# Performance work log

Hardware: AMD Instinct MI355X
Metric: run time of the kernel (lower is better)

Reference implementation:

```python
import jax, jax.numpy as jnp
import numpy as np

N, D, K = 32768, 128, 32
EPS = 1e-8  # torch.cosine_similarity default eps


def setup_inputs() -> dict:
    key = jax.random.key(0)
    k1, k2, k3, k4, k5 = jax.random.split(key, 5)
    # xavier_normal_ std = sqrt(2/(fan_in+fan_out)); torch treats dims (-2,-1) as (fan_in, fan_out)
    std_w = (2.0 / (D + D)) ** 0.5
    std_v = (2.0 / (2 * D + 1)) ** 0.5
    return {
        "x_1": jax.random.normal(k1, (N, D), dtype=jnp.float32),
        "x_2": jax.random.normal(k2, (N, D), dtype=jnp.float32),
        "W1": jax.random.normal(k3, (K, D, D), dtype=jnp.float32) * std_w,
        "W2": jax.random.normal(k4, (K, D, D), dtype=jnp.float32) * std_w,
        "V": jax.random.normal(k5, (K, 2 * D, 1), dtype=jnp.float32) * std_v,
        "b": jnp.zeros((K,), dtype=jnp.float32),
    }


def reference(x_1, x_2, W1, W2, V, b):
    # Batched bilinear transforms: [N, K, D]
    x1t = jnp.einsum("nd,kde->nke", x_1, W1)
    x2t = jnp.einsum("nd,kde->nke", x_2, W2)
    # Cosine similarity along last dim (torch semantics: clamp norms at eps)
    dot = jnp.sum(x1t * x2t, axis=-1)                     # [N, K]
    n1 = jnp.maximum(jnp.linalg.norm(x1t, axis=-1), EPS)  # [N, K]
    n2 = jnp.maximum(jnp.linalg.norm(x2t, axis=-1), EPS)
    part1 = dot / (n1 * n2)
    # part2 = cat([x1, x2]) @ V[k]  -> [N, K]
    xcat = jnp.concatenate([x_1, x_2], axis=-1)           # [N, 2D]
    part2 = jnp.einsum("nf,kf->nk", xcat, V[:, :, 0])
    return jax.nn.relu(part1 + part2 + b)
```

## Files before the change

### kernel.cpp

```cpp
#include <hip/hip_runtime.h>
#include <cstdint>
#include <cstddef>

#define DD 128
#define KK 32
constexpr float EPS = 1e-8f;

typedef __bf16 bf16x8 __attribute__((ext_vector_type(8)));
typedef float f32x4 __attribute__((ext_vector_type(4)));

__device__ __forceinline__ unsigned short f2bf(float x) {
    union { float f; uint32_t u; } v; v.f = x;
    uint32_t r = v.u + 0x7FFFu + ((v.u >> 16) & 1u);
    return (unsigned short)(r >> 16);
}
__device__ __forceinline__ __bf16 f2bf16(float x) {
    unsigned short u = f2bf(x);
    __bf16 r; __builtin_memcpy(&r, &u, 2); return r;
}
__device__ __forceinline__ uint4 pack8(float4 a, float4 b) {
    uint4 o;
    o.x = (uint32_t)f2bf(a.x) | ((uint32_t)f2bf(a.y) << 16);
    o.y = (uint32_t)f2bf(a.z) | ((uint32_t)f2bf(a.w) << 16);
    o.z = (uint32_t)f2bf(b.x) | ((uint32_t)f2bf(b.y) << 16);
    o.w = (uint32_t)f2bf(b.z) | ((uint32_t)f2bf(b.w) << 16);
    return o;
}

template <int CTRL>
__device__ __forceinline__ float dpp_fold(float x) {
    union { float f; int i; } u, r;
    u.f = x;
    r.i = __builtin_amdgcn_update_dpp(0, u.i, CTRL, 0xF, 0xF, false);
    return x + r.f;
}
__device__ __forceinline__ f32x4 fold4(f32x4 v) {
    #pragma unroll
    for (int c = 0; c < 4; ++c) {
        float x = v[c];
        x = dpp_fold<0xB1>(x);
        x = dpp_fold<0x4E>(x);
        v[c] = x;
    }
    return v;
}

__global__ __launch_bounds__(256) void prep_kernel(
    const float* __restrict__ x1, const float* __restrict__ x2,
    const float* __restrict__ W1, const float* __restrict__ W2,
    __bf16* __restrict__ X1f, __bf16* __restrict__ X2f,
    __bf16* __restrict__ W1f, __bf16* __restrict__ W2f,
    int cvt_half, int wf_half)
{
    __shared__ float tile[16][132];
    int bb = blockIdx.x;
    if (bb < 2 * cvt_half) {
        const float* src; __bf16* dst;
        if (bb >= cvt_half) { src = x2; dst = X2f; bb -= cvt_half; }
        else                { src = x1; dst = X1f; }
        const int rg = bb;
        {
            const int row = threadIdx.x >> 4;
            const int c8  = (threadIdx.x & 15) * 8;
            const float* p = src + (size_t)(rg * 16 + row) * DD + c8;
            float4 f0 = *reinterpret_cast<const float4*>(p);
            float4 f1 = *reinterpret_cast<const float4*>(p + 4);
            *reinterpret_cast<float4*>(&tile[row][c8])     = f0;
            *reinterpret_cast<float4*>(&tile[row][c8 + 4]) = f1;
        }
        __syncthreads();
        {
            const int mm = threadIdx.x & 15;
            const int c  = threadIdx.x >> 4;
            float4 a = *reinterpret_cast<float4*>(&tile[mm][c * 8]);
            float4 b = *reinterpret_cast<float4*>(&tile[mm][c * 8 + 4]);
            size_t off = (size_t)rg * 2048 + (size_t)c * 128 + (size_t)mm * 8;
            *reinterpret_cast<uint4*>(dst + off) = pack8(a, b);
        }
    } else {
        bb -= 2 * cvt_half;
        const float* W; __bf16* Wf;
        if (bb >= wf_half) { W = W2; Wf = W2f; bb -= wf_half; }
        else               { W = W1; Wf = W1f; }
        int idx = bb * 256 + threadIdx.x;
        int mm = idx & 15;
        int c  = (idx >> 4) & 15;
        int eg = (idx >> 8) & 7;
        int k  = idx >> 11;
        const float* Wk = W + (size_t)k * DD * DD;
        int e = eg * 16 + mm;
        float4 a, b;
        a.x = Wk[(size_t)(c * 8 + 0) * DD + e];
        a.y = Wk[(size_t)(c * 8 + 1) * DD + e];
        a.z = Wk[(size_t)(c * 8 + 2) * DD + e];
        a.w = Wk[(size_t)(c * 8 + 3) * DD + e];
        b.x = Wk[(size_t)(c * 8 + 4) * DD + e];
        b.y = Wk[(size_t)(c * 8 + 5) * DD + e];
        b.z = Wk[(size_t)(c * 8 + 6) * DD + e];
        b.w = Wk[(size_t)(c * 8 + 7) * DD + e];
        size_t off = ((size_t)(k * 8 + eg)) * 2048 + (size_t)c * 128 + (size_t)mm * 8;
        *reinterpret_cast<uint4*>(Wf + off) = pack8(a, b);
    }
}

__global__ __launch_bounds__(256, 2) void ntn_main(
    const __bf16* __restrict__ X1f, const __bf16* __restrict__ X2f,
    const __bf16* __restrict__ W1f, const __bf16* __restrict__ W2f,
    const float* __restrict__ V, const float* __restrict__ bias,
    float* __restrict__ out, int grp_per_xcd)
{
    __shared__ __align__(16) float sRedAll[8][3][2][4][40];
    __shared__ __align__(16) float sP2[8][2][2][16];

    const int b    = blockIdx.x;
    const int xcd  = b & 7;
    const int k    = (b >> 3) & 31;
    const int grpN = xcd * grp_per_xcd + (b >> 8);
    const int tid  = threadIdx.x;
    const int wave = tid >> 6;
    const int lane = tid & 63;
    const int m    = lane & 15;
    const int quad = lane >> 4;
    const int rh   = wave & 1;
    const int eh   = wave >> 1;

    const size_t nOut = (size_t)grpN * 256 + tid;
    const float bk  = bias[k];

    const __bf16* W1p = W1f + (size_t)k * 16384;
    const __bf16* W2p = W2f + (size_t)k * 16384;

    bf16x8 Bc[2][4][4];
    #pragma unroll
    for (int ks = 0; ks < 4; ++ks)
        #pragma unroll
        for (int et = 0; et < 4; ++et) {
            const size_t boff = (size_t)(eh * 4 + et) * 2048 + ks * 512 + lane * 8;
            Bc[0][ks][et] = *reinterpret_cast<const bf16x8*>(W1p + boff);
            Bc[1][ks][et] = *reinterpret_cast<const bf16x8*>(W2p + boff);
        }

    bf16x8 Vb[4];
    {
        const float* Vk = V + (size_t)k * 256 + eh * 128 + quad * 8;
        #pragma unroll
        for (int ks = 0; ks < 4; ++ks) {
            float4 v0 = *reinterpret_cast<const float4*>(Vk + ks * 32);
            float4 v1 = *reinterpret_cast<const float4*>(Vk + ks * 32 + 4);
            bf16x8 t;
            t[0] = f2bf16(v0.x); t[1] = f2bf16(v0.y);
            t[2] = f2bf16(v0.z); t[3] = f2bf16(v0.w);
            t[4] = f2bf16(v1.x); t[5] = f2bf16(v1.y);
            t[6] = f2bf16(v1.z); t[7] = f2bf16(v1.w);
            if (m != 0) {
                #pragma unroll
                for (int j = 0; j < 8; ++j) t[j] = (__bf16)0.0f;
            }
            Vb[ks] = t;
        }
    }

    const int rg0 = grpN * 16;
    const size_t lane8 = (size_t)lane * 8;

    bf16x8 a1[4], a2[4];
    {
        const size_t ab = (size_t)(rg0 + rh) * 2048 + lane8;
        #pragma unroll
        for (int ks = 0; ks < 4; ++ks) {
            a1[ks] = *reinterpret_cast<const bf16x8*>(X1f + ab + ks * 512);
            a2[ks] = *reinterpret_cast<const bf16x8*>(X2f + ab + ks * 512);
        }
    }

    #pragma unroll
    for (int g = 0; g < 8; ++g) {
        f32x4 acc[2][4];
        #pragma unroll
        for (int mat = 0; mat < 2; ++mat)
            #pragma unroll
            for (int et = 0; et < 4; ++et) acc[mat][et] = f32x4{0.f, 0.f, 0.f, 0.f};
        f32x4 accv = {0.f, 0.f, 0.f, 0.f};

        __builtin_amdgcn_s_setprio(1);
        #pragma unroll
        for (int ks = 0; ks < 4; ++ks) {
            #pragma unroll
            for (int et = 0; et < 4; ++et) {
                acc[0][et] = __builtin_amdgcn_mfma_f32_16x16x32_bf16(a1[ks], Bc[0][ks][et], acc[0][et], 0, 0, 0);
                acc[1][et] = __builtin_amdgcn_mfma_f32_16x16x32_bf16(a2[ks], Bc[1][ks][et], acc[1][et], 0, 0, 0);
            }
        }
        if (eh == 0) {
            #pragma unroll
            for (int ks = 0; ks < 4; ++ks)
                accv = __builtin_amdgcn_mfma_f32_16x16x32_bf16(a1[ks], Vb[ks], accv, 0, 0, 0);
        } else {
            #pragma unroll
            for (int ks = 0; ks < 4; ++ks)
                accv = __builtin_amdgcn_mfma_f32_16x16x32_bf16(a2[ks], Vb[ks], accv, 0, 0, 0);
        }
        __builtin_amdgcn_s_setprio(0);

        if (g < 7) {
            const size_t ab = (size_t)(rg0 + (g + 1) * 2 + rh) * 2048 + lane8;
            #pragma unroll
            for (int ks = 0; ks < 4; ++ks) {
                a1[ks] = *reinterpret_cast<const bf16x8*>(X1f + ab + ks * 512);
                a2[ks] = *reinterpret_cast<const bf16x8*>(X2f + ab + ks * 512);
            }
        }

        f32x4 pd = {0.f, 0.f, 0.f, 0.f};
        f32x4 q1 = {0.f, 0.f, 0.f, 0.f};
        f32x4 q2 = {0.f, 0.f, 0.f, 0.f};
        #pragma unroll
        for (int et = 0; et < 4; ++et) {
            f32x4 c1 = acc[0][et];
            f32x4 c2 = acc[1][et];
            pd += c1 * c2;
            q1 += c1 * c1;
            q2 += c2 * c2;
        }
        pd = fold4(pd);
        q1 = fold4(q1);
        q2 = fold4(q2);

        if ((m & 3) == 0) {
            const int grp = m >> 2;
            const int rb  = rh * 16 + quad * 4;
            *reinterpret_cast<f32x4*>(&sRedAll[g][0][eh][grp][rb]) = pd;
            *reinterpret_cast<f32x4*>(&sRedAll[g][1][eh][grp][rb]) = q1;
            *reinterpret_cast<f32x4*>(&sRedAll[g][2][eh][grp][rb]) = q2;
        }
        if (m == 0) {
            *reinterpret_cast<f32x4*>(&sP2[g][eh][rh][quad * 4]) = accv;
        }
    }

    __syncthreads();

    {
        const int tile = tid >> 5;
        const int row  = tid & 31;
        const int rowh = row >> 4;
        const int rowl = row & 15;
        float dot = 0.f, s1 = 0.f, s2 = 0.f;
        #pragma unroll
        for (int e2 = 0; e2 < 2; ++e2)
            #pragma unroll
            for (int gg = 0; gg < 4; ++gg) {
                dot += sRedAll[tile][0][e2][gg][row];
                s1  += sRedAll[tile][1][e2][gg][row];
                s2  += sRedAll[tile][2][e2][gg][row];
            }
        float p2v = sP2[tile][0][rowh][rowl] + sP2[tile][1][rowh][rowl];
        float n1 = fmaxf(sqrtf(s1), EPS);
        float n2 = fmaxf(sqrtf(s2), EPS);
        float tot = dot / (n1 * n2) + p2v + bk;
        out[nOut * KK + k] = fmaxf(tot, 0.f);
    }
}

extern "C" void kernel_launch(void* const* d_in, const int* in_sizes, int n_in,
                              void* d_out, int out_size, void* d_ws, size_t ws_size,
                              hipStream_t stream) {
    const float* x1 = (const float*)d_in[0];
    const float* x2 = (const float*)d_in[1];
    const float* W1 = (const float*)d_in[2];
    const float* W2 = (const float*)d_in[3];
    const float* V  = (const float*)d_in[4];
    const float* b  = (const float*)d_in[5];
    float* out = (float*)d_out;

    const int N = in_sizes[0] / DD;

    __bf16* X1f = (__bf16*)d_ws;
    __bf16* X2f = X1f + (size_t)N * DD;
    __bf16* W1f = X2f + (size_t)N * DD;
    __bf16* W2f = W1f + (size_t)KK * DD * DD;

    const int cvt_half = N / 16;
    const int wf_half  = KK * DD * DD / 8 / 256;
    prep_kernel<<<2 * cvt_half + 2 * wf_half, 256, 0, stream>>>(
        x1, x2, W1, W2, X1f, X2f, W1f, W2f, cvt_half, wf_half);

    const int groups = N / 256;
    ntn_main<<<groups * KK, 256, 0, stream>>>(X1f, X2f, W1f, W2f, V, b, out,
                                              groups / 8);
}
```

Before: 167.6 us.

## Compute V projection once in prep kernel instead of per-k in main kernel

The concatenated-input projection against V was computed inside the main kernel for every k-block, re-running the same MFMA on each input tile 32 times with only one useful column. It now runs once per 16-row tile in the prep kernel, which writes two partial planes (x1 and x2 halves) of an N×K float buffer that the main kernel reads and sums. This removes MFMA work, V loads and shared-memory traffic from the hot kernel. The cost is an extra global write and read of N×K×2 floats, plus more workspace.

```diff
diff --git a/kernel.cpp b/kernel.cpp
--- a/kernel.cpp
+++ b/kernel.cpp
@@ -48,16 +48,18 @@
 __global__ __launch_bounds__(256) void prep_kernel(
     const float* __restrict__ x1, const float* __restrict__ x2,
     const float* __restrict__ W1, const float* __restrict__ W2,
+    const float* __restrict__ V,
     __bf16* __restrict__ X1f, __bf16* __restrict__ X2f,
     __bf16* __restrict__ W1f, __bf16* __restrict__ W2f,
+    float* __restrict__ p2,
     int cvt_half, int wf_half)
 {
     __shared__ float tile[16][132];
     int bb = blockIdx.x;
     if (bb < 2 * cvt_half) {
-        const float* src; __bf16* dst;
-        if (bb >= cvt_half) { src = x2; dst = X2f; bb -= cvt_half; }
-        else                { src = x1; dst = X1f; }
+        const float* src; __bf16* dst; int half;
+        if (bb >= cvt_half) { src = x2; dst = X2f; half = 1; bb -= cvt_half; }
+        else                { src = x1; dst = X1f; half = 0; }
         const int rg = bb;
         {
             const int row = threadIdx.x >> 4;
@@ -76,6 +78,42 @@
             float4 b = *reinterpret_cast<float4*>(&tile[mm][c * 8 + 4]);
             size_t off = (size_t)rg * 2048 + (size_t)c * 128 + (size_t)mm * 8;
             *reinterpret_cast<uint4*>(dst + off) = pack8(a, b);
+        }
+        const int wave = threadIdx.x >> 6;
+        if (wave < 2) {
+            const int lane = threadIdx.x & 63;
+            const int m    = lane & 15;
+            const int quad = lane >> 4;
+            const int ct   = wave;
+            bf16x8 a[4], bf[4];
+            #pragma unroll
+            for (int ks = 0; ks < 4; ++ks) {
+                float4 a0 = *reinterpret_cast<float4*>(&tile[m][ks * 32 + quad * 8]);
+                float4 a1 = *reinterpret_cast<float4*>(&tile[m][ks * 32 + quad * 8 + 4]);
+                bf16x8 t;
+                t[0] = f2bf16(a0.x); t[1] = f2bf16(a0.y);
+                t[2] = f2bf16(a0.z); t[3] = f2bf16(a0.w);
+                t[4] = f2bf16(a1.x); t[5] = f2bf16(a1.y);
+                t[6] = f2bf16(a1.z); t[7] = f2bf16(a1.w);
+                a[ks] = t;
+                const float* Vp = V + (size_t)(ct * 16 + m) * 256 + half * 128 + ks * 32 + quad * 8;
+                float4 v0 = *reinterpret_cast<const float4*>(Vp);
+                float4 v1 = *reinterpret_cast<const float4*>(Vp + 4);
+                bf16x8 u;
+                u[0] = f2bf16(v0.x); u[1] = f2bf16(v0.y);
+                u[2] = f2bf16(v0.z); u[3] = f2bf16(v0.w);
+                u[4] = f2bf16(v1.x); u[5] = f2bf16(v1.y);
+                u[6] = f2bf16(v1.z); u[7] = f2bf16(v1.w);
+                bf[ks] = u;
+            }
+            f32x4 acc = {0.f, 0.f, 0.f, 0.f};
+            #pragma unroll
+            for (int ks = 0; ks < 4; ++ks)
+                acc = __builtin_amdgcn_mfma_f32_16x16x32_bf16(a[ks], bf[ks], acc, 0, 0, 0);
+            float* p2h = p2 + (size_t)half * (size_t)cvt_half * 16 * KK;
+            #pragma unroll
+            for (int reg = 0; reg < 4; ++reg)
+                p2h[(size_t)(rg * 16 + quad * 4 + reg) * KK + ct * 16 + m] = acc[reg];
         }
     } else {
         bb -= 2 * cvt_half;
@@ -106,11 +144,10 @@
 __global__ __launch_bounds__(256, 2) void ntn_main(
     const __bf16* __restrict__ X1f, const __bf16* __restrict__ X2f,
     const __bf16* __restrict__ W1f, const __bf16* __restrict__ W2f,
-    const float* __restrict__ V, const float* __restrict__ bias,
-    float* __restrict__ out, int grp_per_xcd)
+    const float* __restrict__ p2, const float* __restrict__ bias,
+    float* __restrict__ out, int grp_per_xcd, int plane)
 {
     __shared__ __align__(16) float sRedAll[8][3][2][4][40];
-    __shared__ __align__(16) float sP2[8][2][2][16];
 
     const int b    = blockIdx.x;
     const int xcd  = b & 7;
@@ -125,6 +162,7 @@
     const int eh   = wave >> 1;
 
     const size_t nOut = (size_t)grpN * 256 + tid;
+    const float p2v = p2[nOut * KK + k] + p2[nOut * KK + k + (size_t)plane];
     const float bk  = bias[k];
 
     const __bf16* W1p = W1f + (size_t)k * 16384;
@@ -140,26 +178,6 @@
             Bc[1][ks][et] = *reinterpret_cast<const bf16x8*>(W2p + boff);
         }
 
-    bf16x8 Vb[4];
-    {
-        const float* Vk = V + (size_t)k * 256 + eh * 128 + quad * 8;
-        #pragma unroll
-        for (int ks = 0; ks < 4; ++ks) {
-            float4 v0 = *reinterpret_cast<const float4*>(Vk + ks * 32);
-            float4 v1 = *reinterpret_cast<const float4*>(Vk + ks * 32 + 4);
-            bf16x8 t;
-            t[0] = f2bf16(v0.x); t[1] = f2bf16(v0.y);
-            t[2] = f2bf16(v0.z); t[3] = f2bf16(v0.w);
-            t[4] = f2bf16(v1.x); t[5] = f2bf16(v1.y);
-            t[6] = f2bf16(v1.z); t[7] = f2bf16(v1.w);
-            if (m != 0) {
-                #pragma unroll
-                for (int j = 0; j < 8; ++j) t[j] = (__bf16)0.0f;
-            }
-            Vb[ks] = t;
-        }
-    }
-
     const int rg0 = grpN * 16;
     const size_t lane8 = (size_t)lane * 8;
 
@@ -180,7 +198,6 @@
         for (int mat = 0; mat < 2; ++mat)
             #pragma unroll
             for (int et = 0; et < 4; ++et) acc[mat][et] = f32x4{0.f, 0.f, 0.f, 0.f};
-        f32x4 accv = {0.f, 0.f, 0.f, 0.f};
 
         __builtin_amdgcn_s_setprio(1);
         #pragma unroll
@@ -190,15 +207,6 @@
                 acc[0][et] = __builtin_amdgcn_mfma_f32_16x16x32_bf16(a1[ks], Bc[0][ks][et], acc[0][et], 0, 0, 0);
                 acc[1][et] = __builtin_amdgcn_mfma_f32_16x16x32_bf16(a2[ks], Bc[1][ks][et], acc[1][et], 0, 0, 0);
             }
-        }
-        if (eh == 0) {
-            #pragma unroll
-            for (int ks = 0; ks < 4; ++ks)
-                accv = __builtin_amdgcn_mfma_f32_16x16x32_bf16(a1[ks], Vb[ks], accv, 0, 0, 0);
-        } else {
-            #pragma unroll
-            for (int ks = 0; ks < 4; ++ks)
-                accv = __builtin_amdgcn_mfma_f32_16x16x32_bf16(a2[ks], Vb[ks], accv, 0, 0, 0);
         }
         __builtin_amdgcn_s_setprio(0);
 
@@ -233,9 +241,6 @@
             *reinterpret_cast<f32x4*>(&sRedAll[g][1][eh][grp][rb]) = q1;
             *reinterpret_cast<f32x4*>(&sRedAll[g][2][eh][grp][rb]) = q2;
         }
-        if (m == 0) {
-            *reinterpret_cast<f32x4*>(&sP2[g][eh][rh][quad * 4]) = accv;
-        }
     }
 
     __syncthreads();
@@ -243,8 +248,6 @@
     {
         const int tile = tid >> 5;
         const int row  = tid & 31;
-        const int rowh = row >> 4;
-        const int rowl = row & 15;
         float dot = 0.f, s1 = 0.f, s2 = 0.f;
         #pragma unroll
         for (int e2 = 0; e2 < 2; ++e2)
@@ -254,7 +257,6 @@
                 s1  += sRedAll[tile][1][e2][gg][row];
                 s2  += sRedAll[tile][2][e2][gg][row];
             }
-        float p2v = sP2[tile][0][rowh][rowl] + sP2[tile][1][rowh][rowl];
         float n1 = fmaxf(sqrtf(s1), EPS);
         float n2 = fmaxf(sqrtf(s2), EPS);
         float tot = dot / (n1 * n2) + p2v + bk;
@@ -279,13 +281,14 @@
     __bf16* X2f = X1f + (size_t)N * DD;
     __bf16* W1f = X2f + (size_t)N * DD;
     __bf16* W2f = W1f + (size_t)KK * DD * DD;
+    float*  p2  = (float*)(W2f + (size_t)KK * DD * DD);
 
     const int cvt_half = N / 16;
     const int wf_half  = KK * DD * DD / 8 / 256;
     prep_kernel<<<2 * cvt_half + 2 * wf_half, 256, 0, stream>>>(
-        x1, x2, W1, W2, X1f, X2f, W1f, W2f, cvt_half, wf_half);
+        x1, x2, W1, W2, V, X1f, X2f, W1f, W2f, p2, cvt_half, wf_half);
 
     const int groups = N / 256;
-    ntn_main<<<groups * KK, 256, 0, stream>>>(X1f, X2f, W1f, W2f, V, b, out,
-                                              groups / 8);
-}
+    ntn_main<<<groups * KK, 256, 0, stream>>>(X1f, X2f, W1f, W2f, p2, b, out,
+                                              groups / 8, N * KK);
+}
```

Result: no change. 165.1 us (-1.5%).
